# Performance work log

Measured on AMD Instinct MI355X. Metric: run time of the kernel, lower is better.

The kernel has to match this reference:

```python
import jax, jax.numpy as jnp
import numpy as np
import math

B, S, D = 8, 4096, 128  # batch, seq_len, embed_dim == attention_head_size
EPS = 1e-5


def layer_norm(x, w, b):
    mu = jnp.mean(x, axis=-1, keepdims=True)
    var = jnp.var(x, axis=-1, keepdims=True)
    return (x - mu) * jax.lax.rsqrt(var + EPS) * w + b


def setup_inputs() -> dict:
    key = jax.random.key(0)
    ks = jax.random.split(key, 4)
    x = jax.random.normal(ks[0], (B, S, D), dtype=jnp.float32)
    Wq = jax.random.normal(ks[1], (D, D), dtype=jnp.float32) / math.sqrt(D)
    Wk = jax.random.normal(ks[2], (D, D), dtype=jnp.float32) / math.sqrt(D)
    Wv = jax.random.normal(ks[3], (D, D), dtype=jnp.float32) / math.sqrt(D)
    qn_w = jnp.ones((D,), dtype=jnp.float32)
    qn_b = jnp.zeros((D,), dtype=jnp.float32)
    kn_w = jnp.ones((D,), dtype=jnp.float32)
    kn_b = jnp.zeros((D,), dtype=jnp.float32)
    return {"x": x, "Wq": Wq, "Wk": Wk, "Wv": Wv,
            "qn_w": qn_w, "qn_b": qn_b, "kn_w": kn_w, "kn_b": kn_b}


def reference(x, Wq, Wk, Wv, qn_w, qn_b, kn_w, kn_b):
    # q/k/v projections (nn.Linear with no bias: x @ W^T)
    q = layer_norm(jnp.einsum('bsd,hd->bsh', x, Wq), qn_w, qn_b)
    k = layer_norm(jnp.einsum('bsd,hd->bsh', x, Wk), kn_w, kn_b)
    v = jnp.einsum('bsd,hd->bsh', x, Wv)
    scale = math.sqrt(D)
    scores = jnp.einsum('bqh,bkh->bqk', q, k) / scale  # [B, S, S]
    attn = jax.nn.softmax(scores, axis=-1)
    # dropout_rate = 0.0 -> identity
    return jnp.einsum('bqk,bkh->bqh', attn, v)
```

## Files before the change

kernel.cpp:

```cpp
#include <hip/hip_runtime.h>

#define B_ 8
#define S_ 4096
#define D_ 128
#define KVB 64
#define NT (S_ / KVB)

typedef __attribute__((ext_vector_type(4))) float f32x4;
typedef __attribute__((ext_vector_type(8))) short s16x8;

__device__ __forceinline__ unsigned short f2bf(float f) {
    union { float f; unsigned u; } v; v.f = f;
    unsigned r = (v.u + 0x7fffu + ((v.u >> 16) & 1u)) >> 16;
    return (unsigned short)r;
}

__device__ __forceinline__ unsigned cvt_pk(float lo, float hi) {
    unsigned r;
    asm("v_cvt_pk_bf16_f32 %0, %1, %2" : "=v"(r) : "v"(lo), "v"(hi));
    return r;
}

__device__ __forceinline__ s16x8 load_cvt8(const float* p) {
    f32x4 a = *(const f32x4*)p;
    f32x4 b = *(const f32x4*)(p + 4);
    s16x8 r;
    r[0] = (short)f2bf(a[0]); r[1] = (short)f2bf(a[1]);
    r[2] = (short)f2bf(a[2]); r[3] = (short)f2bf(a[3]);
    r[4] = (short)f2bf(b[0]); r[5] = (short)f2bf(b[1]);
    r[6] = (short)f2bf(b[2]); r[7] = (short)f2bf(b[3]);
    return r;
}

__device__ __forceinline__ void gld16(unsigned short* lds, const unsigned short* g) {
    __builtin_amdgcn_global_load_lds(
        (const __attribute__((address_space(1))) unsigned int*)g,
        (__attribute__((address_space(3))) unsigned int*)lds,
        16, 0, 0);
}

__global__ __launch_bounds__(256, 1) void proj_kernel(
    const float* __restrict__ x,  const float* __restrict__ Wq,
    const float* __restrict__ Wk, const float* __restrict__ Wv,
    const float* __restrict__ qn_w, const float* __restrict__ qn_b,
    const float* __restrict__ kn_w, const float* __restrict__ kn_b,
    unsigned short* __restrict__ qo, unsigned short* __restrict__ ko,
    unsigned short* __restrict__ vto)
{
    __shared__ unsigned short wlds[128 * 136];
    __shared__ unsigned short vstage[128 * 72];

    const int tid  = threadIdx.x;
    const int lane = tid & 63;
    const int wv   = tid >> 6;
    const int j    = lane & 15;
    const int g    = lane >> 4;

    const int b    = blockIdx.x >> 6;
    const int sblk = (blockIdx.x & 63) * 64;
    const int srow = sblk + wv * 16;

    const float* xrow = x + ((size_t)b * S_ + srow + j) * D_;
    s16x8 af[4];
#pragma unroll
    for (int kk = 0; kk < 4; ++kk) af[kk] = load_cvt8(xrow + kk * 32 + g * 8);

    const int wrow = tid >> 1;
    const int wcol = (tid & 1) * 64;

#pragma unroll 1
    for (int m = 0; m < 3; ++m) {
        const float* Wm = (m == 0) ? Wq : (m == 1) ? Wk : Wv;
        __syncthreads();
#pragma unroll
        for (int it = 0; it < 8; ++it) {
            int col = wcol + it * 8;
            *(s16x8*)&wlds[wrow * 136 + col] = load_cvt8(Wm + wrow * 128 + col);
        }
        __syncthreads();

        f32x4 acc[8];
#pragma unroll
        for (int ct = 0; ct < 8; ++ct) { f32x4 z = {0.f, 0.f, 0.f, 0.f}; acc[ct] = z; }
#pragma unroll
        for (int ct = 0; ct < 8; ++ct) {
#pragma unroll
            for (int kk = 0; kk < 4; ++kk) {
                s16x8 bf = *(const s16x8*)&wlds[(ct * 16 + j) * 136 + kk * 32 + g * 8];
                acc[ct] = __builtin_amdgcn_mfma_f32_16x16x32_bf16(af[kk], bf, acc[ct], 0, 0, 0);
            }
        }

        if (m < 2) {
            const float* lw = (m == 0) ? qn_w : kn_w;
            const float* lb = (m == 0) ? qn_b : kn_b;
            float sum[4], sq[4];
#pragma unroll
            for (int r = 0; r < 4; ++r) {
                float s1 = 0.f, s2 = 0.f;
#pragma unroll
                for (int ct = 0; ct < 8; ++ct) { float v = acc[ct][r]; s1 += v; s2 += v * v; }
#pragma unroll
                for (int msk = 1; msk < 16; msk <<= 1) {
                    s1 += __shfl_xor(s1, msk);
                    s2 += __shfl_xor(s2, msk);
                }
                sum[r] = s1; sq[r] = s2;
            }
            float gwv[8], gbv[8];
#pragma unroll
            for (int ct = 0; ct < 8; ++ct) { gwv[ct] = lw[ct * 16 + j]; gbv[ct] = lb[ct * 16 + j]; }
            unsigned short* dst = (m == 0) ? qo : ko;
            const float post = (m == 0) ? 0.12751742361888f : 1.0f;
#pragma unroll
            for (int r = 0; r < 4; ++r) {
                float mean = sum[r] * (1.f / 128.f);
                float var  = sq[r] * (1.f / 128.f) - mean * mean;
                float rstd = rsqrtf(var + 1e-5f);
                size_t rowoff = ((size_t)b * S_ + sblk + wv * 16 + g * 4 + r) * D_;
#pragma unroll
                for (int ct = 0; ct < 8; ++ct) {
                    float val = ((acc[ct][r] - mean) * rstd * gwv[ct] + gbv[ct]) * post;
                    dst[rowoff + ct * 16 + j] = f2bf(val);
                }
            }
        } else {
#pragma unroll
            for (int ct = 0; ct < 8; ++ct) {
#pragma unroll
                for (int r = 0; r < 4; ++r) {
                    vstage[(ct * 16 + j) * 72 + wv * 16 + g * 4 + r] = f2bf(acc[ct][r]);
                }
            }
            __syncthreads();
            int h  = tid >> 1;
            int cb = (tid & 1) * 32;
#pragma unroll
            for (int c = 0; c < 4; ++c) {
                *(s16x8*)(vto + ((size_t)b * D_ + h) * S_ + sblk + cb + c * 8) =
                    *(const s16x8*)&vstage[h * 72 + cb + c * 8];
            }
        }
    }
}

__global__ __launch_bounds__(256, 1) void attn_kernel(
    const unsigned short* __restrict__ qb, const unsigned short* __restrict__ kb,
    const unsigned short* __restrict__ vtb, float* __restrict__ out)
{
    __shared__ unsigned short kbuf[2][KVB * D_];
    __shared__ unsigned short vbuf[2][D_ * KVB];

    const int tid  = threadIdx.x;
    const int lane = tid & 63;
    const int wv   = tid >> 6;
    const int qg   = wv & 1;
    const int kh   = wv >> 1;
    const int j    = lane & 15;
    const int g    = lane >> 4;

    const int swz = (blockIdx.x & 7) * 64 + (blockIdx.x >> 3);
    const int b   = swz >> 6;
    const int s0  = (swz & 63) * 64;

    const unsigned short* qr0 = qb + ((size_t)b * S_ + s0 + qg * 32 + j) * D_;
    const unsigned short* qr1 = qr0 + 16 * D_;
    s16x8 qf0[4], qf1[4];
#pragma unroll
    for (int kk = 0; kk < 4; ++kk) {
        qf0[kk] = *(const s16x8*)(qr0 + kk * 32 + g * 8);
        qf1[kk] = *(const s16x8*)(qr1 + kk * 32 + g * 8);
    }

    const unsigned short* kg_base = kb  + (size_t)b * S_ * D_;
    const unsigned short* vg_base = vtb + (size_t)b * D_ * S_;

    auto STAGE = [&](int bi, int kt) {
        const int kv0 = kt * KVB;
#pragma unroll
        for (int it = 0; it < 4; ++it) {
            const int row = wv * 16 + it * 4 + (lane >> 4);
            const int fk  = (row & 3) | (((row >> 3) & 1) << 2);
            const unsigned short* src =
                kg_base + (size_t)(kv0 + row) * D_ + (((lane & 15) ^ fk) << 3);
            gld16(&kbuf[bi][(wv * 16 + it * 4) * D_], src);
        }
#pragma unroll
        for (int it = 0; it < 4; ++it) {
            const int h = wv * 32 + it * 8 + (lane >> 3);
            const unsigned short* src =
                vg_base + (size_t)h * S_ + kv0 + (((lane & 7) ^ (h & 7)) << 3);
            gld16(&vbuf[bi][(wv * 32 + it * 8) * KVB], src);
        }
    };

    STAGE(0, 0);
    STAGE(1, 1);

    f32x4 acc[2][8];
#pragma unroll
    for (int qs = 0; qs < 2; ++qs)
#pragma unroll
        for (int ht = 0; ht < 8; ++ht) { f32x4 z = {0.f,0.f,0.f,0.f}; acc[qs][ht] = z; }
    f32x4 acc_l[2];
    { f32x4 z = {0.f,0.f,0.f,0.f}; acc_l[0] = z; acc_l[1] = z; }

    s16x8 ones;
#pragma unroll
    for (int e = 0; e < 8; ++e) ones[e] = (short)0x3F80;

    const int fKj   = j & 7;
    const int prow0 = 8 * (j >> 2) + (j & 3) + 32 * kh;
    const int prow1 = prow0 + 4;
    const int vslot = ((4 * kh) ^ 0);

#pragma unroll 1
    for (int kt = 0; kt < NT; ++kt) {
        const int cur = kt & 1;
        if (kt + 1 < NT) { asm volatile("s_waitcnt vmcnt(8)" ::: "memory"); }
        else             { asm volatile("s_waitcnt vmcnt(0)" ::: "memory"); }
        __builtin_amdgcn_s_barrier();
        asm volatile("" ::: "memory");

        const unsigned short* kl = kbuf[cur];
        const unsigned short* vl = vbuf[cur];

        f32x4 sv[2][2];
#pragma unroll
        for (int qs = 0; qs < 2; ++qs) {
            f32x4 z = {0.f,0.f,0.f,0.f}; sv[qs][0] = z; sv[qs][1] = z;
        }
        __builtin_amdgcn_s_setprio(1);
#pragma unroll
        for (int kk = 0; kk < 4; ++kk) {
            const int cs = (((kk * 4 + g) ^ fKj) << 3);
            s16x8 k0 = *(const s16x8*)&kl[prow0 * D_ + cs];
            s16x8 k1 = *(const s16x8*)&kl[prow1 * D_ + cs];
            sv[0][0] = __builtin_amdgcn_mfma_f32_16x16x32_bf16(k0, qf0[kk], sv[0][0], 0, 0, 0);
            sv[1][0] = __builtin_amdgcn_mfma_f32_16x16x32_bf16(k0, qf1[kk], sv[1][0], 0, 0, 0);
            sv[0][1] = __builtin_amdgcn_mfma_f32_16x16x32_bf16(k1, qf0[kk], sv[0][1], 0, 0, 0);
            sv[1][1] = __builtin_amdgcn_mfma_f32_16x16x32_bf16(k1, qf1[kk], sv[1][1], 0, 0, 0);
        }
        __builtin_amdgcn_s_setprio(0);

        float p0[8], p1[8];
#pragma unroll
        for (int r = 0; r < 4; ++r) {
            p0[r]     = exp2f(sv[0][0][r]);
            p0[4 + r] = exp2f(sv[0][1][r]);
            p1[r]     = exp2f(sv[1][0][r]);
            p1[4 + r] = exp2f(sv[1][1][r]);
        }

        union { unsigned u[4]; s16x8 v; } P0, P1;
        P0.u[0] = cvt_pk(p0[0], p0[1]); P0.u[1] = cvt_pk(p0[2], p0[3]);
        P0.u[2] = cvt_pk(p0[4], p0[5]); P0.u[3] = cvt_pk(p0[6], p0[7]);
        P1.u[0] = cvt_pk(p1[0], p1[1]); P1.u[1] = cvt_pk(p1[2], p1[3]);
        P1.u[2] = cvt_pk(p1[4], p1[5]); P1.u[3] = cvt_pk(p1[6], p1[7]);

        __builtin_amdgcn_s_setprio(1);
        acc_l[0] = __builtin_amdgcn_mfma_f32_16x16x32_bf16(P0.v, ones, acc_l[0], 0, 0, 0);
        acc_l[1] = __builtin_amdgcn_mfma_f32_16x16x32_bf16(P1.v, ones, acc_l[1], 0, 0, 0);
#pragma unroll
        for (int ht = 0; ht < 8; ++ht) {
            const int hrow = ht * 16 + j;
            s16x8 vf = *(const s16x8*)&vl[hrow * KVB + (((4 * kh + g) ^ fKj) << 3)];
            acc[0][ht] = __builtin_amdgcn_mfma_f32_16x16x32_bf16(P0.v, vf, acc[0][ht], 0, 0, 0);
            acc[1][ht] = __builtin_amdgcn_mfma_f32_16x16x32_bf16(P1.v, vf, acc[1][ht], 0, 0, 0);
        }
        __builtin_amdgcn_s_setprio(0);

        asm volatile("" ::: "memory");
        __builtin_amdgcn_s_barrier();
        asm volatile("" ::: "memory");
        if (kt + 2 < NT) STAGE(cur, kt + 2);
    }

    float* csum = (float*)&kbuf[0][0];
    float* lsum = (float*)&vbuf[0][0];
    if (kh == 1) {
#pragma unroll
        for (int qs = 0; qs < 2; ++qs) {
#pragma unroll
            for (int ht = 0; ht < 8; ++ht)
                *(f32x4*)&csum[(((qg * 2 + qs) * 8 + ht) * 64 + lane) * 4] = acc[qs][ht];
            *(f32x4*)&lsum[((qg * 2 + qs) * 64 + lane) * 4] = acc_l[qs];
        }
    }
    __syncthreads();
    if (kh == 0) {
#pragma unroll
        for (int qs = 0; qs < 2; ++qs) {
            f32x4 lt = *(const f32x4*)&lsum[((qg * 2 + qs) * 64 + lane) * 4];
            f32x4 li;
#pragma unroll
            for (int r = 0; r < 4; ++r) li[r] = 1.0f / (acc_l[qs][r] + lt[r]);
#pragma unroll
            for (int ht = 0; ht < 8; ++ht) {
                f32x4 o = *(const f32x4*)&csum[(((qg * 2 + qs) * 8 + ht) * 64 + lane) * 4];
                size_t base = ((size_t)b * S_ + s0 + qg * 32 + qs * 16 + g * 4) * D_ + ht * 16 + j;
                out[base         ] = (acc[qs][ht][0] + o[0]) * li[0];
                out[base +     D_] = (acc[qs][ht][1] + o[1]) * li[1];
                out[base + 2 * D_] = (acc[qs][ht][2] + o[2]) * li[2];
                out[base + 3 * D_] = (acc[qs][ht][3] + o[3]) * li[3];
            }
        }
    }
}

extern "C" void kernel_launch(void* const* d_in, const int* in_sizes, int n_in,
                              void* d_out, int out_size, void* d_ws, size_t ws_size,
                              hipStream_t stream) {
    const float* x    = (const float*)d_in[0];
    const float* Wq   = (const float*)d_in[1];
    const float* Wk   = (const float*)d_in[2];
    const float* Wv   = (const float*)d_in[3];
    const float* qn_w = (const float*)d_in[4];
    const float* qn_b = (const float*)d_in[5];
    const float* kn_w = (const float*)d_in[6];
    const float* kn_b = (const float*)d_in[7];
    float* out = (float*)d_out;

    const size_t n = (size_t)B_ * S_ * D_;
    unsigned short* qws  = (unsigned short*)d_ws;
    unsigned short* kws  = qws + n;
    unsigned short* vtws = kws + n;

    proj_kernel<<<512, 256, 0, stream>>>(x, Wq, Wk, Wv, qn_w, qn_b, kn_w, kn_b,
                                         qws, kws, vtws);
    attn_kernel<<<512, 256, 0, stream>>>(qws, kws, vtws, out);
}
```

Baseline: 125.5 us.

## Software-pipeline PV MFMAs one tile behind QK and raise occupancy to two blocks

The P·V MFMAs for tile kt-1 are deferred into iteration kt, issued after the K fragments for kt are loaded from LDS. V fragments are read into registers before the barrier, so the buffer can be restaged while the matrix cores still have work. This is meant to overlap exp/convert and LDS latency with MFMA work. Launch bounds also change to two blocks per CU, which caps registers while vfr and kf add register pressure, so spilling is a risk.

```diff
diff --git a/kernel.cpp b/kernel.cpp
--- a/kernel.cpp
+++ b/kernel.cpp
@@ -144,7 +144,7 @@
     }
 }
 
-__global__ __launch_bounds__(256, 1) void attn_kernel(
+__global__ __launch_bounds__(256, 2) void attn_kernel(
     const unsigned short* __restrict__ qb, const unsigned short* __restrict__ kb,
     const unsigned short* __restrict__ vtb, float* __restrict__ out)
 {
@@ -212,7 +212,22 @@
     const int fKj   = j & 7;
     const int prow0 = 8 * (j >> 2) + (j & 3) + 32 * kh;
     const int prow1 = prow0 + 4;
-    const int vslot = ((4 * kh) ^ 0);
+
+    s16x8 vfr[8];
+    union PU { unsigned u[4]; s16x8 v; };
+    PU P0, P1;
+
+    auto PV_PREV = [&]() {
+        __builtin_amdgcn_s_setprio(1);
+        acc_l[0] = __builtin_amdgcn_mfma_f32_16x16x32_bf16(P0.v, ones, acc_l[0], 0, 0, 0);
+        acc_l[1] = __builtin_amdgcn_mfma_f32_16x16x32_bf16(P1.v, ones, acc_l[1], 0, 0, 0);
+#pragma unroll
+        for (int ht = 0; ht < 8; ++ht) {
+            acc[0][ht] = __builtin_amdgcn_mfma_f32_16x16x32_bf16(P0.v, vfr[ht], acc[0][ht], 0, 0, 0);
+            acc[1][ht] = __builtin_amdgcn_mfma_f32_16x16x32_bf16(P1.v, vfr[ht], acc[1][ht], 0, 0, 0);
+        }
+        __builtin_amdgcn_s_setprio(0);
+    };
 
 #pragma unroll 1
     for (int kt = 0; kt < NT; ++kt) {
@@ -225,6 +240,16 @@
         const unsigned short* kl = kbuf[cur];
         const unsigned short* vl = vbuf[cur];
 
+        s16x8 kf[8];
+#pragma unroll
+        for (int kk = 0; kk < 4; ++kk) {
+            const int cs = (((kk * 4 + g) ^ fKj) << 3);
+            kf[kk * 2 + 0] = *(const s16x8*)&kl[prow0 * D_ + cs];
+            kf[kk * 2 + 1] = *(const s16x8*)&kl[prow1 * D_ + cs];
+        }
+
+        if (kt) PV_PREV();
+
         f32x4 sv[2][2];
 #pragma unroll
         for (int qs = 0; qs < 2; ++qs) {
@@ -233,15 +258,17 @@
         __builtin_amdgcn_s_setprio(1);
 #pragma unroll
         for (int kk = 0; kk < 4; ++kk) {
-            const int cs = (((kk * 4 + g) ^ fKj) << 3);
-            s16x8 k0 = *(const s16x8*)&kl[prow0 * D_ + cs];
-            s16x8 k1 = *(const s16x8*)&kl[prow1 * D_ + cs];
-            sv[0][0] = __builtin_amdgcn_mfma_f32_16x16x32_bf16(k0, qf0[kk], sv[0][0], 0, 0, 0);
-            sv[1][0] = __builtin_amdgcn_mfma_f32_16x16x32_bf16(k0, qf1[kk], sv[1][0], 0, 0, 0);
-            sv[0][1] = __builtin_amdgcn_mfma_f32_16x16x32_bf16(k1, qf0[kk], sv[0][1], 0, 0, 0);
-            sv[1][1] = __builtin_amdgcn_mfma_f32_16x16x32_bf16(k1, qf1[kk], sv[1][1], 0, 0, 0);
+            sv[0][0] = __builtin_amdgcn_mfma_f32_16x16x32_bf16(kf[kk*2+0], qf0[kk], sv[0][0], 0, 0, 0);
+            sv[1][0] = __builtin_amdgcn_mfma_f32_16x16x32_bf16(kf[kk*2+0], qf1[kk], sv[1][0], 0, 0, 0);
+            sv[0][1] = __builtin_amdgcn_mfma_f32_16x16x32_bf16(kf[kk*2+1], qf0[kk], sv[0][1], 0, 0, 0);
+            sv[1][1] = __builtin_amdgcn_mfma_f32_16x16x32_bf16(kf[kk*2+1], qf1[kk], sv[1][1], 0, 0, 0);
         }
         __builtin_amdgcn_s_setprio(0);
+
+#pragma unroll
+        for (int ht = 0; ht < 8; ++ht) {
+            vfr[ht] = *(const s16x8*)&vl[(ht * 16 + j) * KVB + (((4 * kh + g) ^ fKj) << 3)];
+        }
 
         float p0[8], p1[8];
 #pragma unroll
@@ -251,30 +278,18 @@
             p1[r]     = exp2f(sv[1][0][r]);
             p1[4 + r] = exp2f(sv[1][1][r]);
         }
-
-        union { unsigned u[4]; s16x8 v; } P0, P1;
         P0.u[0] = cvt_pk(p0[0], p0[1]); P0.u[1] = cvt_pk(p0[2], p0[3]);
         P0.u[2] = cvt_pk(p0[4], p0[5]); P0.u[3] = cvt_pk(p0[6], p0[7]);
         P1.u[0] = cvt_pk(p1[0], p1[1]); P1.u[1] = cvt_pk(p1[2], p1[3]);
         P1.u[2] = cvt_pk(p1[4], p1[5]); P1.u[3] = cvt_pk(p1[6], p1[7]);
 
-        __builtin_amdgcn_s_setprio(1);
-        acc_l[0] = __builtin_amdgcn_mfma_f32_16x16x32_bf16(P0.v, ones, acc_l[0], 0, 0, 0);
-        acc_l[1] = __builtin_amdgcn_mfma_f32_16x16x32_bf16(P1.v, ones, acc_l[1], 0, 0, 0);
-#pragma unroll
-        for (int ht = 0; ht < 8; ++ht) {
-            const int hrow = ht * 16 + j;
-            s16x8 vf = *(const s16x8*)&vl[hrow * KVB + (((4 * kh + g) ^ fKj) << 3)];
-            acc[0][ht] = __builtin_amdgcn_mfma_f32_16x16x32_bf16(P0.v, vf, acc[0][ht], 0, 0, 0);
-            acc[1][ht] = __builtin_amdgcn_mfma_f32_16x16x32_bf16(P1.v, vf, acc[1][ht], 0, 0, 0);
-        }
-        __builtin_amdgcn_s_setprio(0);
-
-        asm volatile("" ::: "memory");
+        asm volatile("s_waitcnt lgkmcnt(0)" ::: "memory");
         __builtin_amdgcn_s_barrier();
         asm volatile("" ::: "memory");
         if (kt + 2 < NT) STAGE(cur, kt + 2);
     }
+
+    PV_PREV();
 
     float* csum = (float*)&kbuf[0][0];
     float* lsum = (float*)&vbuf[0][0];
```

New measurement: 120.0 us. 1.05x faster.
